# Performance work log

Hardware: AMD Instinct MI355X
Metric: run time of the kernel (lower is better)

The kernel has to match this reference:

```python
import jax, jax.numpy as jnp
import numpy as np

INPLANES = 128
OUTPLANES = 256
N_IN = 400000      # active input voxels
M_OUT = 100000     # active output voxels (avg 4 of 8 children active)
K_OFF = 8          # 2x2x2 filter offsets
EPS = 1e-4         # scn.BatchNormalization default eps


def setup_inputs() -> dict:
    key = jax.random.key(0)
    k1, k2 = jax.random.split(key, 2)
    feats = jax.random.normal(k1, (N_IN, INPLANES), dtype=jnp.float32)
    # scn conv weight: one [Cin, Cout] matrix per filter offset, fan-in scaled init
    W = jax.random.normal(k2, (K_OFF, INPLANES, OUTPLANES), dtype=jnp.float32) / jnp.sqrt(
        float(K_OFF * INPLANES))
    gamma = jnp.ones((OUTPLANES,), dtype=jnp.float32)
    beta = jnp.zeros((OUTPLANES,), dtype=jnp.float32)

    # Rulebook: for each output voxel, the input row feeding each of the 8
    # filter offsets (stride-2/filter-2 => each input hits exactly one slot).
    # Inactive children point at padding row N_IN (zero features).
    rng = np.random.default_rng(0)
    gather_idx = np.full((M_OUT, K_OFF), N_IN, dtype=np.int32)
    active_offs = np.argsort(rng.random((M_OUT, K_OFF)), axis=1)[:, :4]  # 4 active children
    inp_ids = np.arange(N_IN, dtype=np.int32).reshape(M_OUT, 4)
    gather_idx[np.arange(M_OUT)[:, None], active_offs] = inp_ids

    return {"feats": feats, "W": W, "gamma": gamma, "beta": beta,
            "gather_idx": jnp.asarray(gather_idx)}


def reference(feats, W, gamma, beta, gather_idx):
    # pad row so inactive rulebook entries contribute zero
    feats_p = jnp.concatenate(
        [feats, jnp.zeros((1, feats.shape[1]), dtype=feats.dtype)], axis=0)
    # gather-GEMM-scatter sparse conv: sum over the 8 filter offsets
    out = jnp.zeros((gather_idx.shape[0], W.shape[2]), dtype=feats.dtype)
    for k in range(K_OFF):
        out = out + feats_p[gather_idx[:, k]] @ W[k]      # [M, Cout]
    # scn.BatchNormalization over active output sites (training-mode stats)
    mu = jnp.mean(out, axis=0)
    var = jnp.var(out, axis=0)
    y = (out - mu) * jax.lax.rsqrt(var + EPS) * gamma + beta
    return jax.nn.relu(y)
```

## Files before the change

kernel.cpp:

```cpp
#include <hip/hip_runtime.h>
#include <stdint.h>

#define CIN 128
#define COUT 256
#define NIN 400000
#define MOUT 100000
#define KOFFS 8
#define EPSV 1e-4f
#define BM 64
#define NBLK ((MOUT + BM - 1) / BM)
#define THREADS 512

typedef __attribute__((ext_vector_type(8))) short short8;
typedef __attribute__((ext_vector_type(4))) float f32x4;

__device__ __forceinline__ unsigned f2bf_u(float f) {
  union { float f; unsigned u; } v; v.f = f;
  return (v.u + 0x7FFFu + ((v.u >> 16) & 1u)) >> 16;
}

__global__ void prep_kernel(const float* __restrict__ W,
                            unsigned short* __restrict__ Wt) {
  __shared__ unsigned short t[64][257];
  const int s = blockIdx.x;
  const int tid = threadIdx.x;
  const int koff = s >> 1;
  const int cbase = (s & 1) * 64;
  const float* Wk = W + koff * (CIN * COUT);
  #pragma unroll 8
  for (int c = 0; c < 64; ++c)
    t[c][tid] = (unsigned short)f2bf_u(Wk[(cbase + c) * COUT + tid]);
  __syncthreads();
  uint4* dst = (uint4*)((char*)Wt + s * 32768);
  #pragma unroll
  for (int p = 0; p < 8; ++p) {
    int f = p * 256 + tid;
    int wn = f >> 8, rem = f & 255;
    int g = rem >> 6, l = rem & 63;
    int ks = g >> 1, ni = g & 1;
    int n = wn * 32 + ni * 16 + (l & 15);
    int cb = ks * 32 + ((l >> 4) << 3);
    unsigned short e0 = t[cb + 0][n], e1 = t[cb + 1][n];
    unsigned short e2 = t[cb + 2][n], e3 = t[cb + 3][n];
    unsigned short e4 = t[cb + 4][n], e5 = t[cb + 5][n];
    unsigned short e6 = t[cb + 6][n], e7 = t[cb + 7][n];
    uint4 w;
    w.x = (unsigned)e0 | ((unsigned)e1 << 16);
    w.y = (unsigned)e2 | ((unsigned)e3 << 16);
    w.z = (unsigned)e4 | ((unsigned)e5 << 16);
    w.w = (unsigned)e6 | ((unsigned)e7 << 16);
    dst[f] = w;
  }
}

__global__ __launch_bounds__(THREADS, 2) void conv_kernel(
    const float* __restrict__ feats,
    const unsigned short* __restrict__ Wt,
    const int* __restrict__ gidx,
    unsigned short* __restrict__ rawout,
    float* __restrict__ out32,
    float* __restrict__ partial) {
  __shared__ unsigned short Asm[257 * 128];
  __shared__ int IDXs[BM * KOFFS];

  const int tid = threadIdx.x;
  const int lane = tid & 63;
  const int wave = tid >> 6;
  const int row16 = lane & 15;
  const int quad = lane >> 4;
  const long base_m = (long)blockIdx.x * BM;
  const long in_base = 4 * base_m;

  for (int i = tid; i < BM * KOFFS; i += THREADS) {
    long m = base_m + (i >> 3);
    int idx = (m < MOUT) ? gidx[m * KOFFS + (i & 7)] : NIN;
    long li = (long)idx - in_base;
    IDXs[i] = ((unsigned long)li > 255ul) ? 256 : (int)li;
  }
  if (tid < 16) *(uint4*)((char*)Asm + 256 * 256 + tid * 16) = make_uint4(0, 0, 0, 0);

  {
    const float4* f4 = (const float4*)feats + in_base * 32;
    float4 v[16];
    if (in_base + 256 <= NIN) {
      #pragma unroll
      for (int p = 0; p < 16; ++p) v[p] = f4[p * THREADS + tid];
    } else {
      #pragma unroll
      for (int p = 0; p < 16; ++p) {
        int j = p * THREADS + tid;
        v[p] = (in_base + (j >> 5) < NIN) ? f4[j]
                                          : make_float4(0.f, 0.f, 0.f, 0.f);
      }
    }
    #pragma unroll
    for (int p = 0; p < 16; ++p) {
      int j = p * THREADS + tid;
      int row = j >> 5, ch4 = j & 31;
      uint2 w;
      w.x = f2bf_u(v[p].x) | (f2bf_u(v[p].y) << 16);
      w.y = f2bf_u(v[p].z) | (f2bf_u(v[p].w) << 16);
      *(uint2*)((char*)Asm + row * 256 + ((ch4 * 8) ^ ((row & 7) << 4))) = w;
    }
  }
  __syncthreads();

  short8 B0a, B0b, B1a, B1b;
  auto B_LOAD0 = [&](int s) {
    const char* bp = (const char*)Wt + s * 32768 + (wave << 12) + (lane << 4);
    B0a = *(const short8*)(bp);
    B0b = *(const short8*)(bp + 1024);
  };
  auto B_LOAD1 = [&](int s) {
    const char* bp = (const char*)Wt + s * 32768 + (wave << 12) + 2048 + (lane << 4);
    B1a = *(const short8*)(bp);
    B1b = *(const short8*)(bp + 1024);
  };

  f32x4 acc[4][2];
  #pragma unroll
  for (int mi = 0; mi < 4; ++mi)
    #pragma unroll
    for (int ni = 0; ni < 2; ++ni)
      acc[mi][ni] = (f32x4){0.f, 0.f, 0.f, 0.f};

  int li0, li1, li2, li3;
  auto LI_LOAD = [&](int k) {
    li0 = IDXs[(row16) * 8 + k];
    li1 = IDXs[(row16 + 16) * 8 + k];
    li2 = IDXs[(row16 + 32) * 8 + k];
    li3 = IDXs[(row16 + 48) * 8 + k];
  };
  auto AF = [&](int li, int inner) -> short8 {
    return *(const short8*)((const char*)Asm + li * 256 +
                            (inner ^ ((li & 7) << 4)));
  };

  auto MMA0 = [&](int half) {
    const int inner = (half << 7) + (quad << 4);
    short8 a0 = AF(li0, inner), a1 = AF(li1, inner),
           a2 = AF(li2, inner), a3 = AF(li3, inner);
    __builtin_amdgcn_s_setprio(1);
    acc[0][0] = __builtin_amdgcn_mfma_f32_16x16x32_bf16(a0, B0a, acc[0][0], 0, 0, 0);
    acc[0][1] = __builtin_amdgcn_mfma_f32_16x16x32_bf16(a0, B0b, acc[0][1], 0, 0, 0);
    acc[1][0] = __builtin_amdgcn_mfma_f32_16x16x32_bf16(a1, B0a, acc[1][0], 0, 0, 0);
    acc[1][1] = __builtin_amdgcn_mfma_f32_16x16x32_bf16(a1, B0b, acc[1][1], 0, 0, 0);
    acc[2][0] = __builtin_amdgcn_mfma_f32_16x16x32_bf16(a2, B0a, acc[2][0], 0, 0, 0);
    acc[2][1] = __builtin_amdgcn_mfma_f32_16x16x32_bf16(a2, B0b, acc[2][1], 0, 0, 0);
    acc[3][0] = __builtin_amdgcn_mfma_f32_16x16x32_bf16(a3, B0a, acc[3][0], 0, 0, 0);
    acc[3][1] = __builtin_amdgcn_mfma_f32_16x16x32_bf16(a3, B0b, acc[3][1], 0, 0, 0);
    __builtin_amdgcn_s_setprio(0);
  };
  auto MMA1 = [&](int half) {
    const int inner = (half << 7) + 64 + (quad << 4);
    short8 a0 = AF(li0, inner), a1 = AF(li1, inner),
           a2 = AF(li2, inner), a3 = AF(li3, inner);
    __builtin_amdgcn_s_setprio(1);
    acc[0][0] = __builtin_amdgcn_mfma_f32_16x16x32_bf16(a0, B1a, acc[0][0], 0, 0, 0);
    acc[0][1] = __builtin_amdgcn_mfma_f32_16x16x32_bf16(a0, B1b, acc[0][1], 0, 0, 0);
    acc[1][0] = __builtin_amdgcn_mfma_f32_16x16x32_bf16(a1, B1a, acc[1][0], 0, 0, 0);
    acc[1][1] = __builtin_amdgcn_mfma_f32_16x16x32_bf16(a1, B1b, acc[1][1], 0, 0, 0);
    acc[2][0] = __builtin_amdgcn_mfma_f32_16x16x32_bf16(a2, B1a, acc[2][0], 0, 0, 0);
    acc[2][1] = __builtin_amdgcn_mfma_f32_16x16x32_bf16(a2, B1b, acc[2][1], 0, 0, 0);
    acc[3][0] = __builtin_amdgcn_mfma_f32_16x16x32_bf16(a3, B1a, acc[3][0], 0, 0, 0);
    acc[3][1] = __builtin_amdgcn_mfma_f32_16x16x32_bf16(a3, B1b, acc[3][1], 0, 0, 0);
    __builtin_amdgcn_s_setprio(0);
  };

  B_LOAD0(0);
  #pragma unroll
  for (int T = 0; T < 16; ++T) {
    const int k = T >> 1, half = T & 1;
    if (half == 0) LI_LOAD(k);
    B_LOAD1(T);
    MMA0(half);
    if (T + 1 < 16) B_LOAD0(T + 1);
    MMA1(half);
  }

  float sm[2], sq[2];
  sm[0] = sm[1] = sq[0] = sq[1] = 0.f;
  #pragma unroll
  for (int mi = 0; mi < 4; ++mi) {
    #pragma unroll
    for (int rr = 0; rr < 4; ++rr) {
      long m = base_m + (mi << 4) + (quad << 2) + rr;
      bool ok = (m < MOUT);
      #pragma unroll
      for (int ni = 0; ni < 2; ++ni) {
        float v = acc[mi][ni][rr];
        int n = (wave << 5) + (ni << 4) + row16;
        if (ok) {
          if (rawout) rawout[m * COUT + n] = (unsigned short)f2bf_u(v);
          else        out32[m * COUT + n] = v;
        }
        sm[ni] += v;
        sq[ni] += v * v;
      }
    }
  }
  #pragma unroll
  for (int ni = 0; ni < 2; ++ni) {
    sm[ni] += __shfl_xor(sm[ni], 16);
    sm[ni] += __shfl_xor(sm[ni], 32);
    sq[ni] += __shfl_xor(sq[ni], 16);
    sq[ni] += __shfl_xor(sq[ni], 32);
  }
  if (quad == 0) {
    float* pb = partial + (long)blockIdx.x * 512;
    #pragma unroll
    for (int ni = 0; ni < 2; ++ni) {
      int n = (wave << 5) + (ni << 4) + row16;
      pb[n] = sm[ni];
      pb[n + 256] = sq[ni];
    }
  }
}

__global__ void reduce_kernel(const float* __restrict__ partial,
                              float* __restrict__ partial2) {
  const int j = blockIdx.x;
  const int c = threadIdx.x;
  const int b0 = j * 25;
  const int b1 = (b0 + 25 < NBLK) ? b0 + 25 : NBLK;
  float s = 0.f;
  for (int b = b0; b < b1; ++b) s += partial[(long)b * 512 + c];
  partial2[(long)j * 512 + c] = s;
}

__global__ void finalize_kernel(const float* __restrict__ partial2,
                                const float* __restrict__ gamma,
                                const float* __restrict__ beta,
                                float* __restrict__ ss) {
  int n = threadIdx.x;
  float s = 0.f, q = 0.f;
  #pragma unroll
  for (int j = 0; j < 64; ++j) {
    s += partial2[j * 512 + n];
    q += partial2[j * 512 + 256 + n];
  }
  const float inv = 1.0f / (float)MOUT;
  float mu = s * inv;
  float var = q * inv - mu * mu;
  float sc = rsqrtf(var + EPSV) * gamma[n];
  ss[n] = sc;
  ss[n + 256] = beta[n] - mu * sc;
}

__global__ void apply_bf16(const unsigned short* __restrict__ raw,
                           float* __restrict__ out,
                           const float* __restrict__ ss) {
  const int c0 = (threadIdx.x & 31) << 3;
  float scr[8], shr[8];
  #pragma unroll
  for (int j = 0; j < 8; ++j) { scr[j] = ss[c0 + j]; shr[j] = ss[c0 + j + 256]; }
  const long total = (long)MOUT * COUT / 8;
  const uint4* r4 = (const uint4*)raw;
  float4* o4 = (float4*)out;
  union { unsigned u; float f; } t;
  for (long i = (long)blockIdx.x * blockDim.x + threadIdx.x; i < total;
       i += (long)gridDim.x * blockDim.x) {
    uint4 v = r4[i];
    float4 a, b;
    t.u = v.x << 16;        a.x = t.f;
    t.u = v.x & 0xffff0000; a.y = t.f;
    t.u = v.y << 16;        a.z = t.f;
    t.u = v.y & 0xffff0000; a.w = t.f;
    t.u = v.z << 16;        b.x = t.f;
    t.u = v.z & 0xffff0000; b.y = t.f;
    t.u = v.w << 16;        b.z = t.f;
    t.u = v.w & 0xffff0000; b.w = t.f;
    a.x = fmaxf(fmaf(a.x, scr[0], shr[0]), 0.f);
    a.y = fmaxf(fmaf(a.y, scr[1], shr[1]), 0.f);
    a.z = fmaxf(fmaf(a.z, scr[2], shr[2]), 0.f);
    a.w = fmaxf(fmaf(a.w, scr[3], shr[3]), 0.f);
    b.x = fmaxf(fmaf(b.x, scr[4], shr[4]), 0.f);
    b.y = fmaxf(fmaf(b.y, scr[5], shr[5]), 0.f);
    b.z = fmaxf(fmaf(b.z, scr[6], shr[6]), 0.f);
    b.w = fmaxf(fmaf(b.w, scr[7], shr[7]), 0.f);
    o4[2 * i] = a;
    o4[2 * i + 1] = b;
  }
}

__global__ void apply_f32(float* __restrict__ out, const float* __restrict__ ss) {
  __shared__ float sc[256], sh[256];
  sc[threadIdx.x] = ss[threadIdx.x];
  sh[threadIdx.x] = ss[threadIdx.x + 256];
  __syncthreads();
  const long total = (long)MOUT * COUT / 4;
  float4* o4 = (float4*)out;
  for (long i = (long)blockIdx.x * blockDim.x + threadIdx.x; i < total;
       i += (long)gridDim.x * blockDim.x) {
    float4 v = o4[i];
    int c = (int)(i & 63) << 2;
    v.x = fmaxf(fmaf(v.x, sc[c],     sh[c]),     0.f);
    v.y = fmaxf(fmaf(v.y, sc[c + 1], sh[c + 1]), 0.f);
    v.z = fmaxf(fmaf(v.z, sc[c + 2], sh[c + 2]), 0.f);
    v.w = fmaxf(fmaf(v.w, sc[c + 3], sh[c + 3]), 0.f);
    o4[i] = v;
  }
}

extern "C" void kernel_launch(void* const* d_in, const int* in_sizes, int n_in,
                              void* d_out, int out_size, void* d_ws, size_t ws_size,
                              hipStream_t stream) {
  const float* feats = (const float*)d_in[0];
  const float* W     = (const float*)d_in[1];
  const float* gamma = (const float*)d_in[2];
  const float* beta  = (const float*)d_in[3];
  const int*   gidx  = (const int*)d_in[4];
  float* out = (float*)d_out;

  float* ss = (float*)d_ws;
  unsigned short* Wt = (unsigned short*)((char*)d_ws + 4096);
  float* partial  = (float*)((char*)d_ws + 4096 + 524288);
  float* partial2 = (float*)((char*)partial + (size_t)NBLK * 512 * 4);
  size_t raw_off = 4096 + 524288 + (size_t)NBLK * 512 * 4 + 131072;
  raw_off = (raw_off + 255) & ~(size_t)255;
  const size_t RAW_BYTES = (size_t)MOUT * COUT * 2;
  bool bf16raw = ws_size >= raw_off + RAW_BYTES;
  unsigned short* raw = bf16raw ? (unsigned short*)((char*)d_ws + raw_off) : nullptr;

  hipLaunchKernelGGL(prep_kernel, dim3(16), dim3(256), 0, stream, W, Wt);
  hipLaunchKernelGGL(conv_kernel, dim3(NBLK), dim3(THREADS), 0, stream,
                     feats, Wt, gidx, raw, bf16raw ? nullptr : out, partial);
  hipLaunchKernelGGL(reduce_kernel, dim3(64), dim3(512), 0, stream,
                     partial, partial2);
  hipLaunchKernelGGL(finalize_kernel, dim3(1), dim3(256), 0, stream,
                     partial2, gamma, beta, ss);
  if (bf16raw)
    hipLaunchKernelGGL(apply_bf16, dim3(2048), dim3(256), 0, stream, raw, out, ss);
  else
    hipLaunchKernelGGL(apply_f32, dim3(2048), dim3(256), 0, stream, out, ss);
}
```

Before: 137.6 us.

## Retile conv waves to 4x2 grid with 8 N-fragments and reduce stats in LDS

Changes the per-wave tile from 64 rows x 32 columns to 16 rows x 128 columns (4 M-waves x 2 N-waves). Each wave now reads one A fragment per k-step and reuses it across 8 B fragments, which cuts LDS gather reads at the cost of more global/L2 B-fragment loads and more registers. Feature staging now writes 16-byte vectors to LDS, and the index table is padded to a stride of 9 to reduce bank conflicts. Column statistics are reduced across the M-waves in shared memory before a single coalesced partial write. The trade-off is higher register pressure from the P/Q double-buffered B fragments, which may affect occupancy at 2 blocks per CU.

```diff
diff --git a/kernel.cpp b/kernel.cpp
--- a/kernel.cpp
+++ b/kernel.cpp
@@ -40,15 +40,11 @@
     int ks = g >> 1, ni = g & 1;
     int n = wn * 32 + ni * 16 + (l & 15);
     int cb = ks * 32 + ((l >> 4) << 3);
-    unsigned short e0 = t[cb + 0][n], e1 = t[cb + 1][n];
-    unsigned short e2 = t[cb + 2][n], e3 = t[cb + 3][n];
-    unsigned short e4 = t[cb + 4][n], e5 = t[cb + 5][n];
-    unsigned short e6 = t[cb + 6][n], e7 = t[cb + 7][n];
     uint4 w;
-    w.x = (unsigned)e0 | ((unsigned)e1 << 16);
-    w.y = (unsigned)e2 | ((unsigned)e3 << 16);
-    w.z = (unsigned)e4 | ((unsigned)e5 << 16);
-    w.w = (unsigned)e6 | ((unsigned)e7 << 16);
+    w.x = (unsigned)t[cb + 0][n] | ((unsigned)t[cb + 1][n] << 16);
+    w.y = (unsigned)t[cb + 2][n] | ((unsigned)t[cb + 3][n] << 16);
+    w.z = (unsigned)t[cb + 4][n] | ((unsigned)t[cb + 5][n] << 16);
+    w.w = (unsigned)t[cb + 6][n] | ((unsigned)t[cb + 7][n] << 16);
     dst[f] = w;
   }
 }
@@ -61,159 +57,139 @@
     float* __restrict__ out32,
     float* __restrict__ partial) {
   __shared__ unsigned short Asm[257 * 128];
-  __shared__ int IDXs[BM * KOFFS];
+  __shared__ int IDXs[64 * 9 + 8];
 
   const int tid = threadIdx.x;
   const int lane = tid & 63;
   const int wave = tid >> 6;
+  const int wm = wave >> 1;
+  const int wn = wave & 1;
   const int row16 = lane & 15;
   const int quad = lane >> 4;
   const long base_m = (long)blockIdx.x * BM;
   const long in_base = 4 * base_m;
 
-  for (int i = tid; i < BM * KOFFS; i += THREADS) {
-    long m = base_m + (i >> 3);
-    int idx = (m < MOUT) ? gidx[m * KOFFS + (i & 7)] : NIN;
+  {
+    int r = tid >> 3, k = tid & 7;
+    long m = base_m + r;
+    int idx = (m < MOUT) ? gidx[m * KOFFS + k] : NIN;
     long li = (long)idx - in_base;
-    IDXs[i] = ((unsigned long)li > 255ul) ? 256 : (int)li;
+    IDXs[r * 9 + k] = ((unsigned long)li > 255ul) ? 256 : (int)li;
   }
   if (tid < 16) *(uint4*)((char*)Asm + 256 * 256 + tid * 16) = make_uint4(0, 0, 0, 0);
 
   {
     const float4* f4 = (const float4*)feats + in_base * 32;
-    float4 v[16];
-    if (in_base + 256 <= NIN) {
-      #pragma unroll
-      for (int p = 0; p < 16; ++p) v[p] = f4[p * THREADS + tid];
-    } else {
-      #pragma unroll
-      for (int p = 0; p < 16; ++p) {
-        int j = p * THREADS + tid;
-        v[p] = (in_base + (j >> 5) < NIN) ? f4[j]
-                                          : make_float4(0.f, 0.f, 0.f, 0.f);
-      }
-    }
+    const bool full = (in_base + 256 <= NIN);
     #pragma unroll
-    for (int p = 0; p < 16; ++p) {
-      int j = p * THREADS + tid;
-      int row = j >> 5, ch4 = j & 31;
-      uint2 w;
-      w.x = f2bf_u(v[p].x) | (f2bf_u(v[p].y) << 16);
-      w.y = f2bf_u(v[p].z) | (f2bf_u(v[p].w) << 16);
-      *(uint2*)((char*)Asm + row * 256 + ((ch4 * 8) ^ ((row & 7) << 4))) = w;
-    }
-  }
-  __syncthreads();
-
-  short8 B0a, B0b, B1a, B1b;
-  auto B_LOAD0 = [&](int s) {
-    const char* bp = (const char*)Wt + s * 32768 + (wave << 12) + (lane << 4);
-    B0a = *(const short8*)(bp);
-    B0b = *(const short8*)(bp + 1024);
+    for (int p = 0; p < 8; ++p) {
+      int g = p * THREADS + tid;
+      int row = g >> 4, slot = g & 15;
+      float4 a, b;
+      if (full || in_base + row < NIN) { a = f4[2 * g]; b = f4[2 * g + 1]; }
+      else { a = make_float4(0.f,0.f,0.f,0.f); b = a; }
+      uint4 w;
+      w.x = f2bf_u(a.x) | (f2bf_u(a.y) << 16);
+      w.y = f2bf_u(a.z) | (f2bf_u(a.w) << 16);
+      w.z = f2bf_u(b.x) | (f2bf_u(b.y) << 16);
+      w.w = f2bf_u(b.z) | (f2bf_u(b.w) << 16);
+      *(uint4*)((char*)Asm + row * 256 + (((slot) ^ (row & 7)) << 4)) = w;
+    }
+  }
+  __syncthreads();
+
+  const char* Wtc = (const char*)Wt;
+  auto BLD = [&](int s, int ks, int ni) -> short8 {
+    return *(const short8*)(Wtc + s * 32768 + (wn * 4 + (ni >> 1)) * 4096 +
+                            (ks * 2 + (ni & 1)) * 1024 + (lane << 4));
   };
-  auto B_LOAD1 = [&](int s) {
-    const char* bp = (const char*)Wt + s * 32768 + (wave << 12) + 2048 + (lane << 4);
-    B1a = *(const short8*)(bp);
-    B1b = *(const short8*)(bp + 1024);
-  };
-
-  f32x4 acc[4][2];
-  #pragma unroll
-  for (int mi = 0; mi < 4; ++mi)
-    #pragma unroll
-    for (int ni = 0; ni < 2; ++ni)
-      acc[mi][ni] = (f32x4){0.f, 0.f, 0.f, 0.f};
-
-  int li0, li1, li2, li3;
-  auto LI_LOAD = [&](int k) {
-    li0 = IDXs[(row16) * 8 + k];
-    li1 = IDXs[(row16 + 16) * 8 + k];
-    li2 = IDXs[(row16 + 32) * 8 + k];
-    li3 = IDXs[(row16 + 48) * 8 + k];
-  };
-  auto AF = [&](int li, int inner) -> short8 {
+  auto AF = [&](int li, int s, int ks) -> short8 {
+    int inner = ((s & 1) << 7) + (ks << 6) + (quad << 4);
     return *(const short8*)((const char*)Asm + li * 256 +
                             (inner ^ ((li & 7) << 4)));
   };
 
-  auto MMA0 = [&](int half) {
-    const int inner = (half << 7) + (quad << 4);
-    short8 a0 = AF(li0, inner), a1 = AF(li1, inner),
-           a2 = AF(li2, inner), a3 = AF(li3, inner);
-    __builtin_amdgcn_s_setprio(1);
-    acc[0][0] = __builtin_amdgcn_mfma_f32_16x16x32_bf16(a0, B0a, acc[0][0], 0, 0, 0);
-    acc[0][1] = __builtin_amdgcn_mfma_f32_16x16x32_bf16(a0, B0b, acc[0][1], 0, 0, 0);
-    acc[1][0] = __builtin_amdgcn_mfma_f32_16x16x32_bf16(a1, B0a, acc[1][0], 0, 0, 0);
-    acc[1][1] = __builtin_amdgcn_mfma_f32_16x16x32_bf16(a1, B0b, acc[1][1], 0, 0, 0);
-    acc[2][0] = __builtin_amdgcn_mfma_f32_16x16x32_bf16(a2, B0a, acc[2][0], 0, 0, 0);
-    acc[2][1] = __builtin_amdgcn_mfma_f32_16x16x32_bf16(a2, B0b, acc[2][1], 0, 0, 0);
-    acc[3][0] = __builtin_amdgcn_mfma_f32_16x16x32_bf16(a3, B0a, acc[3][0], 0, 0, 0);
-    acc[3][1] = __builtin_amdgcn_mfma_f32_16x16x32_bf16(a3, B0b, acc[3][1], 0, 0, 0);
-    __builtin_amdgcn_s_setprio(0);
-  };
-  auto MMA1 = [&](int half) {
-    const int inner = (half << 7) + 64 + (quad << 4);
-    short8 a0 = AF(li0, inner), a1 = AF(li1, inner),
-           a2 = AF(li2, inner), a3 = AF(li3, inner);
-    __builtin_amdgcn_s_setprio(1);
-    acc[0][0] = __builtin_amdgcn_mfma_f32_16x16x32_bf16(a0, B1a, acc[0][0], 0, 0, 0);
-    acc[0][1] = __builtin_amdgcn_mfma_f32_16x16x32_bf16(a0, B1b, acc[0][1], 0, 0, 0);
-    acc[1][0] = __builtin_amdgcn_mfma_f32_16x16x32_bf16(a1, B1a, acc[1][0], 0, 0, 0);
-    acc[1][1] = __builtin_amdgcn_mfma_f32_16x16x32_bf16(a1, B1b, acc[1][1], 0, 0, 0);
-    acc[2][0] = __builtin_amdgcn_mfma_f32_16x16x32_bf16(a2, B1a, acc[2][0], 0, 0, 0);
-    acc[2][1] = __builtin_amdgcn_mfma_f32_16x16x32_bf16(a2, B1b, acc[2][1], 0, 0, 0);
-    acc[3][0] = __builtin_amdgcn_mfma_f32_16x16x32_bf16(a3, B1a, acc[3][0], 0, 0, 0);
-    acc[3][1] = __builtin_amdgcn_mfma_f32_16x16x32_bf16(a3, B1b, acc[3][1], 0, 0, 0);
-    __builtin_amdgcn_s_setprio(0);
-  };
-
-  B_LOAD0(0);
-  #pragma unroll
-  for (int T = 0; T < 16; ++T) {
-    const int k = T >> 1, half = T & 1;
-    if (half == 0) LI_LOAD(k);
-    B_LOAD1(T);
-    MMA0(half);
-    if (T + 1 < 16) B_LOAD0(T + 1);
-    MMA1(half);
-  }
-
-  float sm[2], sq[2];
-  sm[0] = sm[1] = sq[0] = sq[1] = 0.f;
-  #pragma unroll
-  for (int mi = 0; mi < 4; ++mi) {
+  f32x4 acc[8];
+  #pragma unroll
+  for (int ni = 0; ni < 8; ++ni) acc[ni] = (f32x4){0.f, 0.f, 0.f, 0.f};
+
+  short8 P[8], Q[8];
+  const int myrow9 = (wm * 16 + row16) * 9;
+
+  #pragma unroll
+  for (int ni = 0; ni < 8; ++ni) P[ni] = BLD(0, 0, ni);
+
+  #pragma unroll
+  for (int s = 0; s < 16; ++s) {
+    const int li = IDXs[myrow9 + (s >> 1)];
+    #pragma unroll
+    for (int ni = 0; ni < 8; ++ni) Q[ni] = BLD(s, 1, ni);
+    {
+      short8 a = AF(li, s, 0);
+      __builtin_amdgcn_s_setprio(1);
+      #pragma unroll
+      for (int ni = 0; ni < 8; ++ni)
+        acc[ni] = __builtin_amdgcn_mfma_f32_16x16x32_bf16(a, P[ni], acc[ni], 0, 0, 0);
+      __builtin_amdgcn_s_setprio(0);
+    }
+    if (s + 1 < 16) {
+      #pragma unroll
+      for (int ni = 0; ni < 8; ++ni) P[ni] = BLD(s + 1, 0, ni);
+    }
+    {
+      short8 a = AF(li, s, 1);
+      __builtin_amdgcn_s_setprio(1);
+      #pragma unroll
+      for (int ni = 0; ni < 8; ++ni)
+        acc[ni] = __builtin_amdgcn_mfma_f32_16x16x32_bf16(a, Q[ni], acc[ni], 0, 0, 0);
+      __builtin_amdgcn_s_setprio(0);
+    }
+  }
+
+  float sm[8], sq[8];
+  #pragma unroll
+  for (int ni = 0; ni < 8; ++ni) { sm[ni] = 0.f; sq[ni] = 0.f; }
+  #pragma unroll
+  for (int ni = 0; ni < 8; ++ni) {
     #pragma unroll
     for (int rr = 0; rr < 4; ++rr) {
-      long m = base_m + (mi << 4) + (quad << 2) + rr;
-      bool ok = (m < MOUT);
-      #pragma unroll
-      for (int ni = 0; ni < 2; ++ni) {
-        float v = acc[mi][ni][rr];
-        int n = (wave << 5) + (ni << 4) + row16;
-        if (ok) {
-          if (rawout) rawout[m * COUT + n] = (unsigned short)f2bf_u(v);
-          else        out32[m * COUT + n] = v;
-        }
-        sm[ni] += v;
-        sq[ni] += v * v;
+      long m = base_m + wm * 16 + (quad << 2) + rr;
+      float v = acc[ni][rr];
+      int n = wn * 128 + (ni << 4) + row16;
+      if (m < MOUT) {
+        if (rawout) rawout[m * COUT + n] = (unsigned short)f2bf_u(v);
+        else        out32[m * COUT + n] = v;
       }
-    }
-  }
-  #pragma unroll
-  for (int ni = 0; ni < 2; ++ni) {
+      sm[ni] += v;
+      sq[ni] += v * v;
+    }
+  }
+  #pragma unroll
+  for (int ni = 0; ni < 8; ++ni) {
     sm[ni] += __shfl_xor(sm[ni], 16);
     sm[ni] += __shfl_xor(sm[ni], 32);
     sq[ni] += __shfl_xor(sq[ni], 16);
     sq[ni] += __shfl_xor(sq[ni], 32);
   }
+  __syncthreads();
+  float* S = (float*)Asm;
+  float* Sq = S + 1024;
   if (quad == 0) {
-    float* pb = partial + (long)blockIdx.x * 512;
     #pragma unroll
-    for (int ni = 0; ni < 2; ++ni) {
-      int n = (wave << 5) + (ni << 4) + row16;
-      pb[n] = sm[ni];
-      pb[n + 256] = sq[ni];
-    }
+    for (int ni = 0; ni < 8; ++ni) {
+      int n = wn * 128 + (ni << 4) + row16;
+      S[wm * 256 + n] = sm[ni];
+      Sq[wm * 256 + n] = sq[ni];
+    }
+  }
+  __syncthreads();
+  if (tid < 256) {
+    float s = S[tid] + S[256 + tid] + S[512 + tid] + S[768 + tid];
+    partial[(long)blockIdx.x * 512 + tid] = s;
+  } else {
+    int n = tid - 256;
+    float q = Sq[n] + Sq[256 + n] + Sq[512 + n] + Sq[768 + n];
+    partial[(long)blockIdx.x * 512 + tid] = q;
   }
 }
 
```

Measured after the change: 226.8 us. +64.9%, slower.
